# Kernel tuning notes

Hardware: AMD Instinct MI355X
Metric: run time of the kernel (lower is better)

## Reference

```python
import jax, jax.numpy as jnp
import numpy as np

COMMITMENT_COST = 0.25
NUM_EMBEDDINGS = 512
EMBEDDING_DIM = 64


def setup_inputs() -> dict:
    key = jax.random.key(0)
    k1, k2 = jax.random.split(key)
    B, T = 64, 1024
    inputs = jax.random.normal(k1, (B, T, EMBEDDING_DIM), dtype=jnp.float32)
    # matches nn.Embedding init uniform_(-1/K, 1/K)
    embedding = jax.random.uniform(
        k2, (NUM_EMBEDDINGS, EMBEDDING_DIM), dtype=jnp.float32,
        minval=-1.0 / NUM_EMBEDDINGS, maxval=1.0 / NUM_EMBEDDINGS)
    return {"inputs": inputs, "embedding": embedding}


def reference(inputs, embedding):
    B = inputs.shape[0]
    K, D = embedding.shape
    flat = inputs.reshape(-1, D)  # [N, D]
    # squared-euclidean distances [N, K] (same expansion as torch source)
    distances = (
        jnp.sum(flat * flat, axis=1, keepdims=True)
        + jnp.sum(embedding * embedding, axis=1)
        - 2.0 * flat @ embedding.T
    )
    idx = jnp.argmin(distances, axis=1)  # [N]
    # one-hot @ embedding  ==  gather
    quantized = embedding[idx].reshape(inputs.shape)

    e_latent_loss = jnp.mean((jax.lax.stop_gradient(quantized) - inputs) ** 2)
    q_latent_loss = jnp.mean((quantized - jax.lax.stop_gradient(inputs)) ** 2)
    loss = q_latent_loss + COMMITMENT_COST * e_latent_loss

    # straight-through estimator
    quantized_st = inputs + jax.lax.stop_gradient(quantized - inputs)

    # avg_probs = mean of one-hot encodings == histogram of indices / N
    counts = jax.ops.segment_sum(
        jnp.ones(flat.shape[0], dtype=jnp.float32), idx, num_segments=K)
    avg_probs = counts / flat.shape[0]
    perplexity = jnp.exp(-jnp.sum(avg_probs * jnp.log(avg_probs + 1e-10)))

    indices_for_transformer = idx.reshape(B, -1)
    return loss, quantized_st, perplexity, indices_for_transformer
```

## Files before the change

### kernel.cpp

```cpp
#include <hip/hip_runtime.h>
#include <math.h>

#define D 64
#define K 512
#define BLOCK 256
#define KSLICE 128
#define NSLICES 4


__device__ __forceinline__ float np_sumsq64(const float* v) {
#pragma clang fp contract(off)
    float r[8];
#pragma unroll
    for (int m = 0; m < 8; ++m) r[m] = v[m] * v[m];
#pragma unroll
    for (int i = 8; i < 64; i += 8) {
#pragma unroll
        for (int m = 0; m < 8; ++m) r[m] = r[m] + v[i + m] * v[i + m];
    }
    return ((r[0] + r[1]) + (r[2] + r[3])) + ((r[4] + r[5]) + (r[6] + r[7]));
}

__global__ __launch_bounds__(BLOCK, 4) void vq_scan(
    const float* __restrict__ x, const float* __restrict__ emb,
    float* __restrict__ stash, int N)
{
    __shared__ float4 e_s[KSLICE * (D / 4)];
    __shared__ float se_s[KSLICE];

    const int tid = threadIdx.x;
    const int kbase = blockIdx.y * KSLICE;

    const float4* esrc = (const float4*)(emb + (size_t)kbase * D);
#pragma unroll
    for (int i = 0; i < (KSLICE * D / 4) / BLOCK; ++i)
        e_s[tid + i * BLOCK] = esrc[tid + i * BLOCK];

    if (tid < KSLICE) {
        float er[D];
        const float4* e4 = (const float4*)(emb + (size_t)(kbase + tid) * D);
#pragma unroll
        for (int j = 0; j < D / 4; ++j) {
            float4 v = e4[j];
            er[4 * j + 0] = v.x; er[4 * j + 1] = v.y;
            er[4 * j + 2] = v.z; er[4 * j + 3] = v.w;
        }
        se_s[tid] = np_sumsq64(er);
    }
    __syncthreads();

    const int row = blockIdx.x * BLOCK + tid;
    if (row >= N) return;

    float xr[D];
    {
        const float4* xp = (const float4*)(x + (size_t)row * D);
#pragma unroll
        for (int j = 0; j < D / 4; ++j) {
            float4 v = xp[j];
            xr[4 * j + 0] = v.x; xr[4 * j + 1] = v.y;
            xr[4 * j + 2] = v.z; xr[4 * j + 3] = v.w;
        }
    }
    const float sx = np_sumsq64(xr);

    float bestd = INFINITY;
    int bi = 0;
    for (int k = 0; k < KSLICE; k += 2) {
        float a0 = 0.f, a1 = 0.f;
        const float4* e0 = &e_s[k * (D / 4)];
        const float4* e1 = &e_s[(k + 1) * (D / 4)];
#pragma unroll
        for (int j = 0; j < D / 4; ++j) {
            float4 ea = e0[j];
            float4 eb = e1[j];
            a0 = fmaf(xr[4 * j + 0], ea.x, a0);
            a1 = fmaf(xr[4 * j + 0], eb.x, a1);
            a0 = fmaf(xr[4 * j + 1], ea.y, a0);
            a1 = fmaf(xr[4 * j + 1], eb.y, a1);
            a0 = fmaf(xr[4 * j + 2], ea.z, a0);
            a1 = fmaf(xr[4 * j + 2], eb.z, a1);
            a0 = fmaf(xr[4 * j + 3], ea.w, a0);
            a1 = fmaf(xr[4 * j + 3], eb.w, a1);
        }
        float d0 = (sx + se_s[k]) - 2.0f * a0;
        float d1 = (sx + se_s[k + 1]) - 2.0f * a1;
        if (d0 < bestd) { bestd = d0; bi = k; }
        if (d1 < bestd) { bestd = d1; bi = k + 1; }
    }

    float2 p; p.x = bestd; p.y = (float)(kbase + bi);
    *(float2*)(stash + (size_t)row * D + 2 * blockIdx.y) = p;
}

__global__ __launch_bounds__(BLOCK) void vq_merge(
    const float* __restrict__ x, const float* __restrict__ emb,
    float* __restrict__ q_out, float* __restrict__ idx_out,
    float* __restrict__ block_sums, int* __restrict__ counts, int N)
{
    __shared__ int hist[K];
    __shared__ float red[BLOCK / 64];
    const int tid = threadIdx.x;
    for (int k = tid; k < K; k += BLOCK) hist[k] = 0;
    __syncthreads();

    const int row = blockIdx.x * BLOCK + tid;
    float s = 0.f;
    if (row < N) {
        float bestd = INFINITY;
        int bi = 0;
#pragma unroll
        for (int sl = 0; sl < NSLICES; ++sl) {
            float2 p = *(const float2*)(q_out + (size_t)row * D + 2 * sl);
            if (p.x < bestd) { bestd = p.x; bi = (int)p.y; }
        }
        atomicAdd(&hist[bi], 1);

        const float4* xp = (const float4*)(x + (size_t)row * D);
        const float4* ep = (const float4*)(emb + (size_t)bi * D);
        float4* qp = (float4*)(q_out + (size_t)row * D);
#pragma unroll
        for (int j = 0; j < D / 4; ++j) {
            float4 xv = xp[j];
            float4 e  = ep[j];
            float dx0 = e.x - xv.x, dx1 = e.y - xv.y;
            float dx2 = e.z - xv.z, dx3 = e.w - xv.w;
            s = fmaf(dx0, dx0, s);
            s = fmaf(dx1, dx1, s);
            s = fmaf(dx2, dx2, s);
            s = fmaf(dx3, dx3, s);
            float4 qs;
            qs.x = xv.x + dx0; qs.y = xv.y + dx1;
            qs.z = xv.z + dx2; qs.w = xv.w + dx3;
            qp[j] = qs;
        }
        idx_out[row] = (float)bi;
    }

    for (int off = 32; off; off >>= 1) s += __shfl_down(s, off, 64);
    if ((tid & 63) == 0) red[tid >> 6] = s;
    __syncthreads();
    if (tid == 0) {
        float t = 0.f;
#pragma unroll
        for (int w = 0; w < BLOCK / 64; ++w) t += red[w];
        block_sums[blockIdx.x] = t;
    }
    for (int k = tid; k < K; k += BLOCK) atomicAdd(&counts[k], hist[k]);
}

__global__ __launch_bounds__(512) void vq_finalize(
    const float* __restrict__ block_sums, int nblocks,
    const int* __restrict__ counts, float* __restrict__ out_loss,
    float* __restrict__ out_perp, float inv_nelem, float inv_rows)
{
    const int tid = threadIdx.x;
    double ls = 0.0;
    for (int i = tid; i < nblocks; i += 512) ls += (double)block_sums[i];
    double ps = 0.0;
    {
        float p = (float)counts[tid] * inv_rows;
        ps = (double)(p * logf(p + 1e-10f));
    }
    for (int off = 32; off; off >>= 1) {
        ls += __shfl_down(ls, off, 64);
        ps += __shfl_down(ps, off, 64);
    }
    __shared__ double l8[8], p8[8];
    if ((tid & 63) == 0) { l8[tid >> 6] = ls; p8[tid >> 6] = ps; }
    __syncthreads();
    if (tid == 0) {
        double L = 0.0, P = 0.0;
#pragma unroll
        for (int w = 0; w < 8; ++w) { L += l8[w]; P += p8[w]; }
        *out_loss = 1.25f * (float)(L * (double)inv_nelem);
        *out_perp = expf((float)(-P));
    }
}

extern "C" void kernel_launch(void* const* d_in, const int* in_sizes, int n_in,
                              void* d_out, int out_size, void* d_ws, size_t ws_size,
                              hipStream_t stream) {
    const float* x   = (const float*)d_in[0];
    const float* emb = (const float*)d_in[1];
    const int N = in_sizes[0] / D;
    const int nblocks = (N + BLOCK - 1) / BLOCK;

    float* out      = (float*)d_out;
    float* loss_out = out;
    float* q_out    = out + 1;
    float* perp_out = out + 1 + (size_t)N * D;
    float* idx_out  = perp_out + 1;

    float* block_sums = (float*)d_ws;
    int*   counts     = (int*)((char*)d_ws + (((size_t)nblocks * 4 + 255) & ~(size_t)255));

    hipMemsetAsync(counts, 0, K * sizeof(int), stream);
    dim3 sgrid(nblocks, NSLICES);
    vq_scan<<<sgrid, BLOCK, 0, stream>>>(x, emb, q_out, N);
    vq_merge<<<nblocks, BLOCK, 0, stream>>>(x, emb, q_out, idx_out,
                                            block_sums, counts, N);
    vq_finalize<<<1, 512, 0, stream>>>(block_sums, nblocks, counts,
                                       loss_out, perp_out,
                                       1.0f / (float)((size_t)N * D),
                                       1.0f / (float)N);
}
```

Baseline: 162.1 us.

## Register-tile scan over two rows and 16 codes, split merge across half-rows

The scan kernel now has each thread handle two rows and keep 16 codebook dot-product accumulators in registers. It streams x from global memory per float4 chunk instead of holding the whole row in registers, and each shared-memory codebook load is reused across both rows. The codebook is split into 8 slices of 64 codes. The merge kernel uses two threads per row, each handling half the columns, skips zero histogram atomics, and grows its grid. This aims to raise FMA-to-LDS ratio and parallelism, at the cost of re-reading x from global per sub-tile and a larger stash-merge per row.

```diff
diff --git a/kernel.cpp b/kernel.cpp
--- a/kernel.cpp
+++ b/kernel.cpp
@@ -4,19 +4,29 @@
 #define D 64
 #define K 512
 #define BLOCK 256
-#define KSLICE 128
-#define NSLICES 4
-
-
-__device__ __forceinline__ float np_sumsq64(const float* v) {
+#define NSLICES 8
+#define KSLICE 64
+#define SUBK 16
+#define RT 2
+
+
+__device__ __forceinline__ float np_sumsq64_g(const float* v) {
 #pragma clang fp contract(off)
     float r[8];
-#pragma unroll
-    for (int m = 0; m < 8; ++m) r[m] = v[m] * v[m];
-#pragma unroll
-    for (int i = 8; i < 64; i += 8) {
-#pragma unroll
-        for (int m = 0; m < 8; ++m) r[m] = r[m] + v[i + m] * v[i + m];
+    {
+        float4 a = *(const float4*)(v + 0);
+        float4 b = *(const float4*)(v + 4);
+        r[0] = a.x * a.x; r[1] = a.y * a.y; r[2] = a.z * a.z; r[3] = a.w * a.w;
+        r[4] = b.x * b.x; r[5] = b.y * b.y; r[6] = b.z * b.z; r[7] = b.w * b.w;
+    }
+#pragma unroll
+    for (int i = 1; i < 8; ++i) {
+        float4 a = *(const float4*)(v + i * 8 + 0);
+        float4 b = *(const float4*)(v + i * 8 + 4);
+        r[0] = r[0] + a.x * a.x; r[1] = r[1] + a.y * a.y;
+        r[2] = r[2] + a.z * a.z; r[3] = r[3] + a.w * a.w;
+        r[4] = r[4] + b.x * b.x; r[5] = r[5] + b.y * b.y;
+        r[6] = r[6] + b.z * b.z; r[7] = r[7] + b.w * b.w;
     }
     return ((r[0] + r[1]) + (r[2] + r[3])) + ((r[4] + r[5]) + (r[6] + r[7]));
 }
@@ -35,62 +45,58 @@
 #pragma unroll
     for (int i = 0; i < (KSLICE * D / 4) / BLOCK; ++i)
         e_s[tid + i * BLOCK] = esrc[tid + i * BLOCK];
-
-    if (tid < KSLICE) {
-        float er[D];
-        const float4* e4 = (const float4*)(emb + (size_t)(kbase + tid) * D);
-#pragma unroll
-        for (int j = 0; j < D / 4; ++j) {
-            float4 v = e4[j];
-            er[4 * j + 0] = v.x; er[4 * j + 1] = v.y;
-            er[4 * j + 2] = v.z; er[4 * j + 3] = v.w;
+    if (tid < KSLICE)
+        se_s[tid] = np_sumsq64_g(emb + (size_t)(kbase + tid) * D);
+    __syncthreads();
+
+    const int r0 = blockIdx.x * (BLOCK * RT) + tid;
+    const int r1 = r0 + BLOCK;
+    const bool v0 = r0 < N, v1 = r1 < N;
+
+    const float4* xa = (const float4*)(x + (size_t)r0 * D);
+    const float4* xb = (const float4*)(x + (size_t)r1 * D);
+    const float sx0 = v0 ? np_sumsq64_g(x + (size_t)r0 * D) : 0.f;
+    const float sx1 = v1 ? np_sumsq64_g(x + (size_t)r1 * D) : 0.f;
+
+    float best0 = INFINITY, best1 = INFINITY;
+    int bi0 = 0, bi1 = 0;
+
+    for (int ks = 0; ks < KSLICE; ks += SUBK) {
+        float a0[SUBK], a1[SUBK];
+#pragma unroll
+        for (int kk = 0; kk < SUBK; ++kk) { a0[kk] = 0.f; a1[kk] = 0.f; }
+
+#pragma unroll 1
+        for (int j4 = 0; j4 < D / 4; ++j4) {
+            float4 xv0 = v0 ? xa[j4] : make_float4(0.f, 0.f, 0.f, 0.f);
+            float4 xv1 = v1 ? xb[j4] : make_float4(0.f, 0.f, 0.f, 0.f);
+#pragma unroll
+            for (int kk = 0; kk < SUBK; ++kk) {
+                float4 e = e_s[(ks + kk) * (D / 4) + j4];
+                a0[kk] = fmaf(xv0.x, e.x, a0[kk]);
+                a0[kk] = fmaf(xv0.y, e.y, a0[kk]);
+                a0[kk] = fmaf(xv0.z, e.z, a0[kk]);
+                a0[kk] = fmaf(xv0.w, e.w, a0[kk]);
+                a1[kk] = fmaf(xv1.x, e.x, a1[kk]);
+                a1[kk] = fmaf(xv1.y, e.y, a1[kk]);
+                a1[kk] = fmaf(xv1.z, e.z, a1[kk]);
+                a1[kk] = fmaf(xv1.w, e.w, a1[kk]);
+            }
         }
-        se_s[tid] = np_sumsq64(er);
-    }
-    __syncthreads();
-
-    const int row = blockIdx.x * BLOCK + tid;
-    if (row >= N) return;
-
-    float xr[D];
-    {
-        const float4* xp = (const float4*)(x + (size_t)row * D);
-#pragma unroll
-        for (int j = 0; j < D / 4; ++j) {
-            float4 v = xp[j];
-            xr[4 * j + 0] = v.x; xr[4 * j + 1] = v.y;
-            xr[4 * j + 2] = v.z; xr[4 * j + 3] = v.w;
+#pragma unroll
+        for (int kk = 0; kk < SUBK; ++kk) {
+            float se = se_s[ks + kk];
+            float d0 = (sx0 + se) - 2.0f * a0[kk];
+            float d1 = (sx1 + se) - 2.0f * a1[kk];
+            if (d0 < best0) { best0 = d0; bi0 = kbase + ks + kk; }
+            if (d1 < best1) { best1 = d1; bi1 = kbase + ks + kk; }
         }
     }
-    const float sx = np_sumsq64(xr);
-
-    float bestd = INFINITY;
-    int bi = 0;
-    for (int k = 0; k < KSLICE; k += 2) {
-        float a0 = 0.f, a1 = 0.f;
-        const float4* e0 = &e_s[k * (D / 4)];
-        const float4* e1 = &e_s[(k + 1) * (D / 4)];
-#pragma unroll
-        for (int j = 0; j < D / 4; ++j) {
-            float4 ea = e0[j];
-            float4 eb = e1[j];
-            a0 = fmaf(xr[4 * j + 0], ea.x, a0);
-            a1 = fmaf(xr[4 * j + 0], eb.x, a1);
-            a0 = fmaf(xr[4 * j + 1], ea.y, a0);
-            a1 = fmaf(xr[4 * j + 1], eb.y, a1);
-            a0 = fmaf(xr[4 * j + 2], ea.z, a0);
-            a1 = fmaf(xr[4 * j + 2], eb.z, a1);
-            a0 = fmaf(xr[4 * j + 3], ea.w, a0);
-            a1 = fmaf(xr[4 * j + 3], eb.w, a1);
-        }
-        float d0 = (sx + se_s[k]) - 2.0f * a0;
-        float d1 = (sx + se_s[k + 1]) - 2.0f * a1;
-        if (d0 < bestd) { bestd = d0; bi = k; }
-        if (d1 < bestd) { bestd = d1; bi = k + 1; }
-    }
-
-    float2 p; p.x = bestd; p.y = (float)(kbase + bi);
-    *(float2*)(stash + (size_t)row * D + 2 * blockIdx.y) = p;
+
+    if (v0) { float2 p; p.x = best0; p.y = (float)bi0;
+              *(float2*)(stash + (size_t)r0 * D + 2 * blockIdx.y) = p; }
+    if (v1) { float2 p; p.x = best1; p.y = (float)bi1;
+              *(float2*)(stash + (size_t)r1 * D + 2 * blockIdx.y) = p; }
 }
 
 __global__ __launch_bounds__(BLOCK) void vq_merge(
@@ -99,28 +105,41 @@
     float* __restrict__ block_sums, int* __restrict__ counts, int N)
 {
     __shared__ int hist[K];
+    __shared__ int bi_s[128];
     __shared__ float red[BLOCK / 64];
     const int tid = threadIdx.x;
+    const int r = tid & 127, h = tid >> 7;
+    const int row = blockIdx.x * 128 + r;
+
     for (int k = tid; k < K; k += BLOCK) hist[k] = 0;
     __syncthreads();
 
-    const int row = blockIdx.x * BLOCK + tid;
+    if (h == 0 && row < N) {
+        const float* sp = q_out + (size_t)row * D;
+        float4 s0 = *(const float4*)(sp + 0);
+        float4 s1 = *(const float4*)(sp + 4);
+        float4 s2 = *(const float4*)(sp + 8);
+        float4 s3 = *(const float4*)(sp + 12);
+        float best = INFINITY; int bi = 0;
+        float dv[8] = { s0.x, s0.z, s1.x, s1.z, s2.x, s2.z, s3.x, s3.z };
+        float kv[8] = { s0.y, s0.w, s1.y, s1.w, s2.y, s2.w, s3.y, s3.w };
+#pragma unroll
+        for (int sl = 0; sl < 8; ++sl)
+            if (dv[sl] < best) { best = dv[sl]; bi = (int)kv[sl]; }
+        bi_s[r] = bi;
+        idx_out[row] = (float)bi;
+        atomicAdd(&hist[bi], 1);
+    }
+    __syncthreads();
+
     float s = 0.f;
     if (row < N) {
-        float bestd = INFINITY;
-        int bi = 0;
-#pragma unroll
-        for (int sl = 0; sl < NSLICES; ++sl) {
-            float2 p = *(const float2*)(q_out + (size_t)row * D + 2 * sl);
-            if (p.x < bestd) { bestd = p.x; bi = (int)p.y; }
-        }
-        atomicAdd(&hist[bi], 1);
-
-        const float4* xp = (const float4*)(x + (size_t)row * D);
-        const float4* ep = (const float4*)(emb + (size_t)bi * D);
-        float4* qp = (float4*)(q_out + (size_t)row * D);
-#pragma unroll
-        for (int j = 0; j < D / 4; ++j) {
+        const int bi = bi_s[r];
+        const float4* xp = (const float4*)(x + (size_t)row * D) + h * 8;
+        const float4* ep = (const float4*)(emb + (size_t)bi * D) + h * 8;
+        float4* qp = (float4*)(q_out + (size_t)row * D) + h * 8;
+#pragma unroll
+        for (int j = 0; j < 8; ++j) {
             float4 xv = xp[j];
             float4 e  = ep[j];
             float dx0 = e.x - xv.x, dx1 = e.y - xv.y;
@@ -134,7 +153,6 @@
             qs.z = xv.z + dx2; qs.w = xv.w + dx3;
             qp[j] = qs;
         }
-        idx_out[row] = (float)bi;
     }
 
     for (int off = 32; off; off >>= 1) s += __shfl_down(s, off, 64);
@@ -146,7 +164,10 @@
         for (int w = 0; w < BLOCK / 64; ++w) t += red[w];
         block_sums[blockIdx.x] = t;
     }
-    for (int k = tid; k < K; k += BLOCK) atomicAdd(&counts[k], hist[k]);
+    for (int k = tid; k < K; k += BLOCK) {
+        int hk = hist[k];
+        if (hk) atomicAdd(&counts[k], hk);
+    }
 }
 
 __global__ __launch_bounds__(512) void vq_finalize(
@@ -184,7 +205,8 @@
     const float* x   = (const float*)d_in[0];
     const float* emb = (const float*)d_in[1];
     const int N = in_sizes[0] / D;
-    const int nblocks = (N + BLOCK - 1) / BLOCK;
+    const int nScanRB  = (N + BLOCK * RT - 1) / (BLOCK * RT);
+    const int nMergeB  = (N + 127) / 128;
 
     float* out      = (float*)d_out;
     float* loss_out = out;
@@ -193,14 +215,14 @@
     float* idx_out  = perp_out + 1;
 
     float* block_sums = (float*)d_ws;
-    int*   counts     = (int*)((char*)d_ws + (((size_t)nblocks * 4 + 255) & ~(size_t)255));
+    int*   counts     = (int*)((char*)d_ws + (((size_t)nMergeB * 4 + 255) & ~(size_t)255));
 
     hipMemsetAsync(counts, 0, K * sizeof(int), stream);
-    dim3 sgrid(nblocks, NSLICES);
+    dim3 sgrid(nScanRB, NSLICES);
     vq_scan<<<sgrid, BLOCK, 0, stream>>>(x, emb, q_out, N);
-    vq_merge<<<nblocks, BLOCK, 0, stream>>>(x, emb, q_out, idx_out,
+    vq_merge<<<nMergeB, BLOCK, 0, stream>>>(x, emb, q_out, idx_out,
                                             block_sums, counts, N);
-    vq_finalize<<<1, 512, 0, stream>>>(block_sums, nblocks, counts,
+    vq_finalize<<<1, 512, 0, stream>>>(block_sums, nMergeB, counts,
                                        loss_out, perp_out,
                                        1.0f / (float)((size_t)N * D),
                                        1.0f / (float)N);
```

Result: slower. 217.8 us (+34.3%).
